# Optimization experiments

Measured on AMD Instinct MI355X. Metric: run time of the kernel, lower is better.

The kernel has to match this reference:

```python
import jax, jax.numpy as jnp
import numpy as np

M = 262144          # total lanes
N_GROUPS = 32768    # unique obstacle ids (static; original uses torch.unique)
H = 64              # lane_hidden_size
I = 64              # lane_info_enc_size
F = 64              # lane_future_enc_size
SOFT_ARGMAX_DEGREE = 1.0


def setup_inputs() -> dict:
    key = jax.random.key(0)
    k = jax.random.split(key, 8)
    lane_ht = jax.random.normal(k[0], (M, H), jnp.float32)
    lane_info_enc = jax.random.normal(k[1], (M, I), jnp.float32)
    lane_future_enc = jax.random.normal(k[2], (M, F), jnp.float32)
    # sorted group ids covering every group (8 lanes per obstacle)
    same_obstacle_mask = jnp.sort(jnp.arange(M, dtype=jnp.int32) % N_GROUPS).reshape(M, 1)
    # lane_scoring_mlp params: Linear(128->16) + ReLU + Linear(16->1)
    W1 = jax.random.normal(k[3], (H + I, 16), jnp.float32) * 0.05
    b1 = jnp.zeros((16,), jnp.float32)
    W2 = jax.random.normal(k[4], (16, 1), jnp.float32) * 0.05
    b2 = jnp.zeros((1,), jnp.float32)
    return {"lane_ht": lane_ht, "lane_info_enc": lane_info_enc,
            "lane_future_enc": lane_future_enc,
            "W1": W1, "b1": b1, "W2": W2, "b2": b2,
            "same_obstacle_mask": same_obstacle_mask}


def reference(lane_ht, lane_info_enc, lane_future_enc, W1, b1, W2, b2, same_obstacle_mask):
    seg = same_obstacle_mask.reshape(-1)                       # [M] int group ids
    # per-lane score via small MLP
    x = jnp.concatenate([lane_ht, lane_info_enc], axis=1)      # [M, 128]
    h = jax.nn.relu(x @ W1 + b1)                               # [M, 16]
    score = (h @ W2 + b2).reshape(-1) * SOFT_ARGMAX_DEGREE     # [M]
    # per-group (segment) softmax -- exact math of the dense MxN min/max/exp/sum emulation
    smax = jax.lax.stop_gradient(
        jax.ops.segment_max(score, seg, num_segments=N_GROUPS))  # [N]
    e = jnp.exp(score - smax[seg])                             # [M]
    denom = jax.ops.segment_sum(e, seg, num_segments=N_GROUPS)  # [N]
    prob = e / denom[seg]                                      # [M]
    # softmax-weighted per-group pooling of concatenated encodings
    total = jnp.concatenate([lane_ht, lane_info_enc, lane_future_enc], axis=1)  # [M, 192]
    return jax.ops.segment_sum(total * prob[:, None], seg, num_segments=N_GROUPS)  # [N, 192]
```

## Files before the change

kernel.cpp:

```cpp
#include <hip/hip_runtime.h>


__global__ __launch_bounds__(256, 3) void lane_attn_kernel(
    const float* __restrict__ ht,
    const float* __restrict__ info,
    const float* __restrict__ fut,
    const float* __restrict__ W1,
    const float* __restrict__ b1,
    const float* __restrict__ W2,
    const float* __restrict__ b2,
    const int*   __restrict__ seg,
    float*       __restrict__ out)
{
    const int tid  = threadIdx.x;
    const int t    = tid & 63;
    const int w    = __builtin_amdgcn_readfirstlane(tid >> 6);
    const int base = blockIdx.x * 64;

    __shared__ float4 xtile[64 * 32];
    __shared__ float  hpart[4][64][20];

#pragma unroll
    for (int i = 0; i < 8; ++i) {
        const int g   = i * 256 + tid;
        const int row = g >> 5;
        const int s   = g & 31;
        const float* src = (s < 16)
            ? (ht   + (size_t)(base + row) * 64 + s * 4)
            : (info + (size_t)(base + row) * 64 + (s - 16) * 4);
        xtile[row * 32 + (s ^ (row & 31))] = *(const float4*)src;
    }
    __syncthreads();

    float h[16];
#pragma unroll
    for (int j = 0; j < 16; ++j) h[j] = 0.0f;

    const float* w1 = W1 + (w * 32) * 16;
#pragma unroll
    for (int k = 0; k < 8; ++k) {
        const int s  = w * 8 + k;
        const float4 v = xtile[t * 32 + (s ^ (t & 31))];
#pragma unroll
        for (int j = 0; j < 16; ++j) {
            h[j] = fmaf(v.x, w1[(k * 4 + 0) * 16 + j], h[j]);
            h[j] = fmaf(v.y, w1[(k * 4 + 1) * 16 + j], h[j]);
            h[j] = fmaf(v.z, w1[(k * 4 + 2) * 16 + j], h[j]);
            h[j] = fmaf(v.w, w1[(k * 4 + 3) * 16 + j], h[j]);
        }
    }
#pragma unroll
    for (int j4 = 0; j4 < 4; ++j4)
        *(float4*)&hpart[w][t][j4 * 4] =
            make_float4(h[j4*4], h[j4*4+1], h[j4*4+2], h[j4*4+3]);
    __syncthreads();

    float score = b2[0];
    {
        float acc[16];
#pragma unroll
        for (int j = 0; j < 16; ++j) acc[j] = b1[j];
#pragma unroll
        for (int ww = 0; ww < 4; ++ww) {
#pragma unroll
            for (int j4 = 0; j4 < 4; ++j4) {
                const float4 p = *(const float4*)&hpart[ww][t][j4 * 4];
                acc[j4*4+0] += p.x; acc[j4*4+1] += p.y;
                acc[j4*4+2] += p.z; acc[j4*4+3] += p.w;
            }
        }
#pragma unroll
        for (int j = 0; j < 16; ++j)
            score = fmaf(fmaxf(acc[j], 0.0f), W2[j], score);
    }

    float m = score;
    m = fmaxf(m, __shfl_xor(m, 1));
    m = fmaxf(m, __shfl_xor(m, 2));
    m = fmaxf(m, __shfl_xor(m, 4));
    float e = __expf(score - m);
    float s8 = e;
    s8 += __shfl_xor(s8, 1);
    s8 += __shfl_xor(s8, 2);
    s8 += __shfl_xor(s8, 4);
    const float prob = e / s8;

    for (int gg = 0; gg < 2; ++gg) {
        const int g2  = w * 2 + gg;
        const int r0  = g2 * 8;
        const int gid = seg[base + r0];
        float a0 = 0.0f, a1 = 0.0f, a2 = 0.0f;
#pragma unroll
        for (int i = 0; i < 8; ++i) {
            const int   r  = r0 + i;
            const float p  = __shfl(prob, r);
            const float* x = (const float*)&xtile[r * 32];
            const int   s0 = ((t >> 2) ^ (r & 31)) * 4 + (t & 3);
            const int   s1 = (((t >> 2) + 16) ^ (r & 31)) * 4 + (t & 3);
            a0 = fmaf(p, x[s0], a0);
            a1 = fmaf(p, x[s1], a1);
            a2 = fmaf(p, fut[(size_t)(base + r) * 64 + t], a2);
        }
        float* o = out + (size_t)gid * 192;
        o[t]       = a0;
        o[64 + t]  = a1;
        o[128 + t] = a2;
    }
}

extern "C" void kernel_launch(void* const* d_in, const int* in_sizes, int n_in,
                              void* d_out, int out_size, void* d_ws, size_t ws_size,
                              hipStream_t stream) {
    const float* ht   = (const float*)d_in[0];
    const float* info = (const float*)d_in[1];
    const float* fut  = (const float*)d_in[2];
    const float* W1   = (const float*)d_in[3];
    const float* b1   = (const float*)d_in[4];
    const float* W2   = (const float*)d_in[5];
    const float* b2   = (const float*)d_in[6];
    const int*   seg  = (const int*)d_in[7];
    float*       out  = (float*)d_out;

    const int M = in_sizes[7];
    const int blocks = M / 64;

    lane_attn_kernel<<<blocks, 256, 0, stream>>>(ht, info, fut, W1, b1, W2, b2,
                                                 seg, out);
}
```

Baseline: 215.2 us.

## Split MLP by hidden unit across 8 waves and prefetch future encodings

Launches 512 threads per block (8 waves) instead of 256. Each wave now computes two of the 16 hidden units over the full 128-dim input rather than a K-slice of all 16, and reduces the partial scores through a small shared array instead of 16-wide partial sums. The future-encoding rows are loaded into registers at kernel start so their latency overlaps the tile load and MLP. Each wave then pools a single group. This cuts register pressure and shared-memory traffic and raises occupancy, at the cost of each wave reading all 32 input vectors and more scalar W1 loads.

```diff
diff --git a/kernel.cpp b/kernel.cpp
--- a/kernel.cpp
+++ b/kernel.cpp
@@ -1,7 +1,7 @@
 #include <hip/hip_runtime.h>
 
 
-__global__ __launch_bounds__(256, 3) void lane_attn_kernel(
+__global__ __launch_bounds__(512, 8) void lane_attn_kernel(
     const float* __restrict__ ht,
     const float* __restrict__ info,
     const float* __restrict__ fut,
@@ -18,11 +18,18 @@
     const int base = blockIdx.x * 64;
 
     __shared__ float4 xtile[64 * 32];
-    __shared__ float  hpart[4][64][20];
+    __shared__ float  spart[8][64];
+
+    float fv[8];
+    {
+        const float* fp = fut + (size_t)(base + w * 8) * 64 + t;
+#pragma unroll
+        for (int i = 0; i < 8; ++i) fv[i] = fp[i * 64];
+    }
 
 #pragma unroll
-    for (int i = 0; i < 8; ++i) {
-        const int g   = i * 256 + tid;
+    for (int i = 0; i < 4; ++i) {
+        const int g   = i * 512 + tid;
         const int row = g >> 5;
         const int s   = g & 31;
         const float* src = (s < 16)
@@ -32,47 +39,30 @@
     }
     __syncthreads();
 
-    float h[16];
+    {
+        float h0 = 0.0f, h1 = 0.0f;
+        const int j0 = 2 * w;
 #pragma unroll
-    for (int j = 0; j < 16; ++j) h[j] = 0.0f;
-
-    const float* w1 = W1 + (w * 32) * 16;
-#pragma unroll
-    for (int k = 0; k < 8; ++k) {
-        const int s  = w * 8 + k;
-        const float4 v = xtile[t * 32 + (s ^ (t & 31))];
-#pragma unroll
-        for (int j = 0; j < 16; ++j) {
-            h[j] = fmaf(v.x, w1[(k * 4 + 0) * 16 + j], h[j]);
-            h[j] = fmaf(v.y, w1[(k * 4 + 1) * 16 + j], h[j]);
-            h[j] = fmaf(v.z, w1[(k * 4 + 2) * 16 + j], h[j]);
-            h[j] = fmaf(v.w, w1[(k * 4 + 3) * 16 + j], h[j]);
+        for (int s = 0; s < 32; ++s) {
+            const float4 v  = xtile[t * 32 + (s ^ (t & 31))];
+            const int    d0 = s * 4;
+            h0 = fmaf(v.x, W1[(d0 + 0) * 16 + j0], h0);
+            h1 = fmaf(v.x, W1[(d0 + 0) * 16 + j0 + 1], h1);
+            h0 = fmaf(v.y, W1[(d0 + 1) * 16 + j0], h0);
+            h1 = fmaf(v.y, W1[(d0 + 1) * 16 + j0 + 1], h1);
+            h0 = fmaf(v.z, W1[(d0 + 2) * 16 + j0], h0);
+            h1 = fmaf(v.z, W1[(d0 + 2) * 16 + j0 + 1], h1);
+            h0 = fmaf(v.w, W1[(d0 + 3) * 16 + j0], h0);
+            h1 = fmaf(v.w, W1[(d0 + 3) * 16 + j0 + 1], h1);
         }
+        spart[w][t] = fmaxf(h0 + b1[j0], 0.0f) * W2[j0]
+                    + fmaxf(h1 + b1[j0 + 1], 0.0f) * W2[j0 + 1];
     }
-#pragma unroll
-    for (int j4 = 0; j4 < 4; ++j4)
-        *(float4*)&hpart[w][t][j4 * 4] =
-            make_float4(h[j4*4], h[j4*4+1], h[j4*4+2], h[j4*4+3]);
     __syncthreads();
 
     float score = b2[0];
-    {
-        float acc[16];
 #pragma unroll
-        for (int j = 0; j < 16; ++j) acc[j] = b1[j];
-#pragma unroll
-        for (int ww = 0; ww < 4; ++ww) {
-#pragma unroll
-            for (int j4 = 0; j4 < 4; ++j4) {
-                const float4 p = *(const float4*)&hpart[ww][t][j4 * 4];
-                acc[j4*4+0] += p.x; acc[j4*4+1] += p.y;
-                acc[j4*4+2] += p.z; acc[j4*4+3] += p.w;
-            }
-        }
-#pragma unroll
-        for (int j = 0; j < 16; ++j)
-            score = fmaf(fmaxf(acc[j], 0.0f), W2[j], score);
-    }
+    for (int ww = 0; ww < 8; ++ww) score += spart[ww][t];
 
     float m = score;
     m = fmaxf(m, __shfl_xor(m, 1));
@@ -85,21 +75,19 @@
     s8 += __shfl_xor(s8, 4);
     const float prob = e / s8;
 
-    for (int gg = 0; gg < 2; ++gg) {
-        const int g2  = w * 2 + gg;
-        const int r0  = g2 * 8;
-        const int gid = seg[base + r0];
+    {
+        const int gid = seg[base + w * 8];
+        const float* xs = (const float*)xtile;
         float a0 = 0.0f, a1 = 0.0f, a2 = 0.0f;
 #pragma unroll
         for (int i = 0; i < 8; ++i) {
-            const int   r  = r0 + i;
-            const float p  = __shfl(prob, r);
-            const float* x = (const float*)&xtile[r * 32];
-            const int   s0 = ((t >> 2) ^ (r & 31)) * 4 + (t & 3);
-            const int   s1 = (((t >> 2) + 16) ^ (r & 31)) * 4 + (t & 3);
-            a0 = fmaf(p, x[s0], a0);
-            a1 = fmaf(p, x[s1], a1);
-            a2 = fmaf(p, fut[(size_t)(base + r) * 64 + t], a2);
+            const int   r = w * 8 + i;
+            const float p = __shfl(prob, r);
+            const int  sH = (((t >> 2)     ) ^ (r & 31)) * 4 + (t & 3);
+            const int  sI = (((t >> 2) + 16) ^ (r & 31)) * 4 + (t & 3);
+            a0 = fmaf(p, xs[r * 128 + sH], a0);
+            a1 = fmaf(p, xs[r * 128 + sI], a1);
+            a2 = fmaf(p, fv[i], a2);
         }
         float* o = out + (size_t)gid * 192;
         o[t]       = a0;
@@ -124,6 +112,6 @@
     const int M = in_sizes[7];
     const int blocks = M / 64;
 
-    lane_attn_kernel<<<blocks, 256, 0, stream>>>(ht, info, fut, W1, b1, W2, b2,
+    lane_attn_kernel<<<blocks, 512, 0, stream>>>(ht, info, fut, W1, b1, W2, b2,
                                                  seg, out);
 }
```

Result: slower. 219.5 us (+2.0%).
